# Performance work log

Hardware: AMD Instinct MI355X
Metric: run time of the kernel (lower is better)

## Reference

```python
import jax, jax.numpy as jnp
import numpy as np

HEADS = 8
DIM_HEAD = 64
SCALE = DIM_HEAD ** -0.5


def setup_inputs() -> dict:
    key = jax.random.key(0)
    ks = jax.random.split(key, 8)
    B, Nq, Dq = 4, 2048, 512
    Nk, Dc = 1024, 768
    inner = HEADS * DIM_HEAD  # 512
    x = jax.random.normal(ks[0], (B, Nq, Dq), dtype=jnp.float32)
    context = jax.random.normal(ks[1], (B, Nk, Dc), dtype=jnp.float32)
    # Linear weights stored [in, out]; y = x @ W (+ b)
    Wq = jax.random.normal(ks[2], (Dq, inner), dtype=jnp.float32) / np.sqrt(Dq)
    Wk = jax.random.normal(ks[3], (Dc, inner), dtype=jnp.float32) / np.sqrt(Dc)
    Wv = jax.random.normal(ks[4], (Dc, inner), dtype=jnp.float32) / np.sqrt(Dc)
    Wo = jax.random.normal(ks[5], (inner, Dq), dtype=jnp.float32) / np.sqrt(inner)
    bo = jax.random.normal(ks[6], (Dq,), dtype=jnp.float32) * 0.01
    return {"x": x, "context": context, "Wq": Wq, "Wk": Wk, "Wv": Wv, "Wo": Wo, "bo": bo}


def reference(x, context, Wq, Wk, Wv, Wo, bo):
    B, Nq, _ = x.shape
    Nk = context.shape[1]
    # projections
    q = x @ Wq          # [B, Nq, h*d]
    k = context @ Wk    # [B, Nk, h*d]
    v = context @ Wv    # [B, Nk, h*d]
    # split heads: b n (h d) -> b h n d
    q = q.reshape(B, Nq, HEADS, DIM_HEAD).transpose(0, 2, 1, 3)
    k = k.reshape(B, Nk, HEADS, DIM_HEAD).transpose(0, 2, 1, 3)
    v = v.reshape(B, Nk, HEADS, DIM_HEAD).transpose(0, 2, 1, 3)
    # fp32 QK^T (ATTN_PRECISION == 'fp32' path)
    sim = jnp.einsum('bhid,bhjd->bhij', q.astype(jnp.float32), k.astype(jnp.float32)) * SCALE
    attn = jax.nn.softmax(sim, axis=-1)
    out = jnp.einsum('bhij,bhjd->bhid', attn, v)  # [B, h, Nq, d]
    out = out.transpose(0, 2, 1, 3).reshape(B, Nq, HEADS * DIM_HEAD)
    return out @ Wo + bo  # dropout=0 -> identity
```

## Files before the change

kernel.cpp:

```cpp
#include <hip/hip_runtime.h>
#include <cstddef>
#include <cstdint>

typedef __attribute__((ext_vector_type(8))) short bf16x8;
typedef __attribute__((ext_vector_type(4))) float f32x4;

static __device__ __forceinline__ short f2bf(float f) {
    union { float f; unsigned u; } x;
    x.f = f;
    unsigned r = (x.u + 0x7FFFu + ((x.u >> 16) & 1u)) >> 16;
    return (short)r;
}

typedef __attribute__((address_space(3))) unsigned lds_u;
typedef const __attribute__((address_space(1))) unsigned glb_u;
static __device__ __forceinline__ void gld_lds16(const void* g, void* l) {
    __builtin_amdgcn_global_load_lds((glb_u*)g, (lds_u*)l, 16, 0, 0);
}

__global__ __launch_bounds__(256) void convert_kernel(
    const float* __restrict__ x, const float* __restrict__ c,
    short* __restrict__ xb, short* __restrict__ cb, int n1, int n2)
{
    int i = blockIdx.x * 256 + threadIdx.x;
    int nn1 = n1 >> 2;
    const float* src; short* dst; int off;
    if (i < nn1) { src = x; dst = xb; off = i; }
    else { src = c; dst = cb; off = i - nn1; if (off >= (n2 >> 2)) return; }
    float4 v = ((const float4*)src)[off];
    ushort4 w;
    w.x = (unsigned short)f2bf(v.x); w.y = (unsigned short)f2bf(v.y);
    w.z = (unsigned short)f2bf(v.z); w.w = (unsigned short)f2bf(v.w);
    ((ushort4*)dst)[off] = w;
}

__global__ __launch_bounds__(256) void wtrans_kernel(
    const float* __restrict__ Wq, const float* __restrict__ Wk,
    const float* __restrict__ Wv, const float* __restrict__ Wo,
    short* __restrict__ wqT, short* __restrict__ wkvT, short* __restrict__ woT)
{
    __shared__ float T[32][33];
    const int z = blockIdx.z;
    const float* src; short* dst; int R;
    if (z == 0)      { src = Wq; dst = wqT;  R = 512; }
    else if (z == 1) { src = Wk; dst = wkvT; R = 768; }
    else if (z == 2) { src = Wv; dst = wkvT + (size_t)512 * 768; R = 768; }
    else             { src = Wo; dst = woT;  R = 512; }
    const int yt = blockIdx.y;
    if (yt * 32 >= R) return;
    const int xt = blockIdx.x;
    const int tid = threadIdx.x;
    {
        int r = tid >> 3, c4 = (tid & 7) * 4;
        float4 v = *(const float4*)&src[(size_t)(yt * 32 + r) * 512 + xt * 32 + c4];
        T[r][c4] = v.x; T[r][c4 + 1] = v.y; T[r][c4 + 2] = v.z; T[r][c4 + 3] = v.w;
    }
    __syncthreads();
    {
        int cc = tid >> 3, r4 = (tid & 7) * 4;
        ushort4 w;
        w.x = (unsigned short)f2bf(T[r4][cc]);     w.y = (unsigned short)f2bf(T[r4 + 1][cc]);
        w.z = (unsigned short)f2bf(T[r4 + 2][cc]); w.w = (unsigned short)f2bf(T[r4 + 3][cc]);
        *(ushort4*)&dst[(size_t)(xt * 32 + cc) * R + yt * 32 + r4] = w;
    }
}

__global__ __launch_bounds__(256) void vtrans_kernel(
    const short* __restrict__ v, short* __restrict__ vT)
{
    __shared__ short T[32][33];
    const int b = blockIdx.z, yt = blockIdx.y, xt = blockIdx.x;
    const int tid = threadIdx.x;
    {
        int r = tid >> 3, c4 = (tid & 7) * 4;
        ushort4 vv = *(const ushort4*)&v[((size_t)(b * 1024 + yt * 32 + r)) * 1024 + xt * 32 + c4];
        T[r][c4] = (short)vv.x; T[r][c4 + 1] = (short)vv.y;
        T[r][c4 + 2] = (short)vv.z; T[r][c4 + 3] = (short)vv.w;
    }
    __syncthreads();
    {
        int cc = tid >> 3, r4 = (tid & 7) * 4;
        ushort4 w;
        w.x = (unsigned short)T[r4][cc];     w.y = (unsigned short)T[r4 + 1][cc];
        w.z = (unsigned short)T[r4 + 2][cc]; w.w = (unsigned short)T[r4 + 3][cc];
        int kk = yt * 32 + r4;
        int kl = kk & 63;
        int g  = ((kl >> 5) << 2) | ((kl >> 2) & 3);
        int p  = (kk & ~63) | (g << 3) | (((kl >> 4) & 1) << 2);
        *(ushort4*)&vT[((size_t)(b * 512 + xt * 32 + cc)) * 1024 + p] = w;
    }
}

static __device__ __forceinline__ void gemm_core(
    const short* __restrict__ A, const short* __restrict__ BT, int K,
    int bm, int bn, short* As, short* Bs, f32x4 acc[4][4])
{
    const int tid  = threadIdx.x;
    const int lane = tid & 63;
    const int wave = tid >> 6;
    const int lm   = lane & 15;
    const int quad = lane >> 4;
    const int wm = (wave >> 1) * 64;
    const int wn = (wave & 1) * 64;
    const int c = tid >> 7, r = tid & 127;

    {
        const short* Ag = &A[(size_t)(bm + r) * K];
        const short* Bg = &BT[(size_t)(bn + r) * K];
        gld_lds16(Ag + c * 8,       &As[tid * 8]);
        gld_lds16(Ag + (c + 2) * 8, &As[(tid + 256) * 8]);
        gld_lds16(Bg + c * 8,       &Bs[tid * 8]);
        gld_lds16(Bg + (c + 2) * 8, &Bs[(tid + 256) * 8]);
    }

    for (int k0 = 0, it = 0; k0 < K; k0 += 32, ++it) {
        short* Ac = As + (it & 1) * 4096;
        short* Bc = Bs + (it & 1) * 4096;
        __syncthreads();
        if (k0 + 32 < K) {
            short* An = As + ((it & 1) ^ 1) * 4096;
            short* Bn = Bs + ((it & 1) ^ 1) * 4096;
            const short* Ag = &A[(size_t)(bm + r) * K + k0 + 32];
            const short* Bg = &BT[(size_t)(bn + r) * K + k0 + 32];
            gld_lds16(Ag + c * 8,       &An[tid * 8]);
            gld_lds16(Ag + (c + 2) * 8, &An[(tid + 256) * 8]);
            gld_lds16(Bg + c * 8,       &Bn[tid * 8]);
            gld_lds16(Bg + (c + 2) * 8, &Bn[(tid + 256) * 8]);
        }
        bf16x8 af[4], bfr[4];
        #pragma unroll
        for (int i = 0; i < 4; ++i)
            af[i] = *(const bf16x8*)&Ac[(quad * 128 + wm + i * 16 + lm) * 8];
        #pragma unroll
        for (int j = 0; j < 4; ++j)
            bfr[j] = *(const bf16x8*)&Bc[(quad * 128 + wn + j * 16 + lm) * 8];
        #pragma unroll
        for (int i = 0; i < 4; ++i)
            #pragma unroll
            for (int j = 0; j < 4; ++j)
                acc[i][j] = __builtin_amdgcn_mfma_f32_16x16x32_bf16(
                    af[i], bfr[j], acc[i][j], 0, 0, 0);
    }
}

__global__ __launch_bounds__(256) void qkv_kernel(
    const short* __restrict__ xb, const short* __restrict__ cb,
    const short* __restrict__ wqT, const short* __restrict__ wkvT,
    short* __restrict__ qb, short* __restrict__ kvb)
{
    __shared__ short As[2 * 4096];
    __shared__ short Bs[2 * 4096];
    const int bid = blockIdx.x;
    const short *A, *BT; short* C; int K, ldc, bm, bn; float cscale;
    if (bid < 256) { A = xb; BT = wqT;  C = qb;  K = 512; ldc = 512;
                     bm = (bid >> 2) * 128; bn = (bid & 3) * 128;
                     cscale = 0.18033688f; }
    else { int b2 = bid - 256; A = cb; BT = wkvT; C = kvb; K = 768; ldc = 1024;
           bm = (b2 >> 3) * 128; bn = (b2 & 7) * 128; cscale = 1.0f; }

    f32x4 acc[4][4] = {};
    gemm_core(A, BT, K, bm, bn, As, Bs, acc);

    const int lane = threadIdx.x & 63, wave = threadIdx.x >> 6;
    const int lm = lane & 15, quad = lane >> 4;
    const int wm = (wave >> 1) * 64, wn = (wave & 1) * 64;
    #pragma unroll
    for (int j = 0; j < 4; ++j) {
        int col = bn + wn + j * 16 + lm;
        #pragma unroll
        for (int i = 0; i < 4; ++i) {
            int row0 = bm + wm + i * 16 + quad * 4;
            #pragma unroll
            for (int r = 0; r < 4; ++r)
                C[(size_t)(row0 + r) * ldc + col] = f2bf(acc[i][j][r] * cscale);
        }
    }
}

__global__ __launch_bounds__(256) void ogemm_kernel(
    const short* __restrict__ ob, const short* __restrict__ woT,
    const float* __restrict__ bias, float* __restrict__ out)
{
    __shared__ short As[2 * 4096];
    __shared__ short Bs[2 * 4096];
    const int bid = blockIdx.x;
    const int bm = (bid >> 2) * 128, bn = (bid & 3) * 128;

    f32x4 acc[4][4] = {};
    gemm_core(ob, woT, 512, bm, bn, As, Bs, acc);

    const int lane = threadIdx.x & 63, wave = threadIdx.x >> 6;
    const int lm = lane & 15, quad = lane >> 4;
    const int wm = (wave >> 1) * 64, wn = (wave & 1) * 64;
    #pragma unroll
    for (int j = 0; j < 4; ++j) {
        int col = bn + wn + j * 16 + lm;
        float bv = bias[col];
        #pragma unroll
        for (int i = 0; i < 4; ++i) {
            int row0 = bm + wm + i * 16 + quad * 4;
            #pragma unroll
            for (int r = 0; r < 4; ++r)
                out[(size_t)(row0 + r) * 512 + col] = acc[i][j][r] + bv;
        }
    }
}

__global__ __launch_bounds__(256) void attn_kernel(
    const short* __restrict__ q, const short* __restrict__ k,
    const short* __restrict__ vT, short* __restrict__ o)
{
    __shared__ short Ks[3 * 4096];
    __shared__ short Vs[3 * 4096];

    const int tid  = threadIdx.x;
    const int lane = tid & 63;
    const int wave = tid >> 6;
    const int lm   = lane & 15;
    const int quad = lane >> 4;

    const int bid = blockIdx.x;
    const int xcdq = bid >> 3;
    const int hb = (bid & 7) + ((xcdq >> 5) << 3);
    const int qt = xcdq & 31;
    const int h = hb & 7, b = hb >> 3;

    const size_t qrow0 = (size_t)b * 2048 + qt * 64;
    const size_t krow0 = (size_t)b * 1024;
    const int hcol = h * 64;
    const size_t vrow0 = ((size_t)b * 8 + h) * 64;

    const short* kg = &k[(krow0 + (tid & 63)) * 1024 + hcol + (tid >> 6) * 8];
    const short* vg = &vT[(vrow0 + (tid & 63)) * 1024 + (tid >> 6) * 8];

    const short* qrow = &q[(qrow0 + wave * 16 + lm) * 512 + hcol];
    bf16x8 qf0 = *(const bf16x8*)&qrow[quad * 8];
    bf16x8 qf1 = *(const bf16x8*)&qrow[32 + quad * 8];
    asm volatile("" :: "v"(qf0), "v"(qf1));

    gld_lds16(kg,      &Ks[tid * 8]);
    gld_lds16(kg + 32, &Ks[(tid + 256) * 8]);
    gld_lds16(vg,      &Vs[tid * 8]);
    gld_lds16(vg + 32, &Vs[(tid + 256) * 8]);
    kg += 64 * 1024; vg += 64;
    gld_lds16(kg,      &Ks[4096 + tid * 8]);
    gld_lds16(kg + 32, &Ks[4096 + (tid + 256) * 8]);
    gld_lds16(vg,      &Vs[4096 + tid * 8]);
    gld_lds16(vg + 32, &Vs[4096 + (tid + 256) * 8]);
    kg += 64 * 1024; vg += 64;

    f32x4 oacc[4] = {};
    float lsum = 0.0f;
    const int fro = (quad * 64 + lm) * 8;

    int ocur = 0;
    int onxt = 2 * 4096;
    for (int t = 0; t < 16; ++t) {
        if (t < 15) asm volatile("s_waitcnt vmcnt(4)" ::: "memory");
        else        asm volatile("s_waitcnt vmcnt(0)" ::: "memory");
        __builtin_amdgcn_s_barrier();
        __builtin_amdgcn_sched_barrier(0);
        if (t < 14) {
            gld_lds16(kg,      &Ks[onxt + tid * 8]);
            gld_lds16(kg + 32, &Ks[onxt + (tid + 256) * 8]);
            gld_lds16(vg,      &Vs[onxt + tid * 8]);
            gld_lds16(vg + 32, &Vs[onxt + (tid + 256) * 8]);
            kg += 64 * 1024; vg += 64;
        }
        const short* Kc = &Ks[ocur + fro];
        const short* Vc = &Vs[ocur + fro];

        f32x4 sacc[4] = {};
        __builtin_amdgcn_s_setprio(1);
        #pragma unroll
        for (int j = 0; j < 4; ++j) {
            bf16x8 kf0 = *(const bf16x8*)&Kc[(j * 16) * 8];
            bf16x8 kf1 = *(const bf16x8*)&Kc[(256 + j * 16) * 8];
            sacc[j] = __builtin_amdgcn_mfma_f32_16x16x32_bf16(kf0, qf0, sacc[j], 0, 0, 0);
            sacc[j] = __builtin_amdgcn_mfma_f32_16x16x32_bf16(kf1, qf1, sacc[j], 0, 0, 0);
        }
        __builtin_amdgcn_s_setprio(0);

        union { unsigned u[4]; bf16x8 v; } pf0, pf1;
        #pragma unroll
        for (int j = 0; j < 4; ++j) {
            #pragma unroll
            for (int rp = 0; rp < 2; ++rp) {
                float p0 = __builtin_amdgcn_exp2f(sacc[j][2 * rp]);
                float p1 = __builtin_amdgcn_exp2f(sacc[j][2 * rp + 1]);
                lsum += p0 + p1;
                unsigned pr;
                asm("v_cvt_pk_bf16_f32 %0, %1, %2" : "=v"(pr) : "v"(p0), "v"(p1));
                if (j < 2) pf0.u[j * 2 + rp] = pr;
                else       pf1.u[(j - 2) * 2 + rp] = pr;
            }
        }

        __builtin_amdgcn_s_setprio(1);
        #pragma unroll
        for (int j = 0; j < 4; ++j) {
            bf16x8 vf0 = *(const bf16x8*)&Vc[(j * 16) * 8];
            bf16x8 vf1 = *(const bf16x8*)&Vc[(256 + j * 16) * 8];
            oacc[j] = __builtin_amdgcn_mfma_f32_16x16x32_bf16(pf0.v, vf0, oacc[j], 0, 0, 0);
            oacc[j] = __builtin_amdgcn_mfma_f32_16x16x32_bf16(pf1.v, vf1, oacc[j], 0, 0, 0);
        }
        __builtin_amdgcn_s_setprio(0);

        ocur += 4096; if (ocur == 12288) ocur = 0;
        onxt += 4096; if (onxt == 12288) onxt = 0;
    }

    float s = lsum;
    s += __shfl_xor(s, 16);
    s += __shfl_xor(s, 32);
    const float inv = 1.0f / s;
    float invr[4];
    #pragma unroll
    for (int r = 0; r < 4; ++r)
        invr[r] = __shfl(inv, quad * 20 + r);

    #pragma unroll
    for (int j = 0; j < 4; ++j) {
        int col = hcol + j * 16 + lm;
        #pragma unroll
        for (int r = 0; r < 4; ++r) {
            size_t row = qrow0 + wave * 16 + quad * 4 + r;
            o[row * 512 + col] = f2bf(oacc[j][r] * invr[r]);
        }
    }
}

extern "C" void kernel_launch(void* const* d_in, const int* in_sizes, int n_in,
                              void* d_out, int out_size, void* d_ws, size_t ws_size,
                              hipStream_t stream)
{
    const float* x   = (const float*)d_in[0];
    const float* ctx = (const float*)d_in[1];
    const float* Wq  = (const float*)d_in[2];
    const float* Wk  = (const float*)d_in[3];
    const float* Wv  = (const float*)d_in[4];
    const float* Wo  = (const float*)d_in[5];
    const float* bo  = (const float*)d_in[6];

    char* ws = (char*)d_ws;
    short* xb   = (short*)(ws);
    short* cb   = (short*)(ws + (8u << 20));
    short* wqT  = (short*)(ws + (14u << 20));
    short* wkvT = (short*)(ws + (14u << 20) + (512u << 10));
    short* woT  = (short*)(ws + (16u << 20));
    short* qb   = (short*)(ws + (16u << 20) + (512u << 10));
    short* kvb  = (short*)(ws + (24u << 20) + (512u << 10));
    short* ob   = xb;
    short* vT   = cb;

    convert_kernel<<<7168, 256, 0, stream>>>(x, ctx, xb, cb, 8192 * 512, 4096 * 768);
    wtrans_kernel<<<dim3(16, 24, 4), 256, 0, stream>>>(Wq, Wk, Wv, Wo, wqT, wkvT, woT);
    qkv_kernel<<<512, 256, 0, stream>>>(xb, cb, wqT, wkvT, qb, kvb);
    vtrans_kernel<<<dim3(16, 32, 4), 256, 0, stream>>>(kvb + 512, vT);
    attn_kernel<<<1024, 256, 0, stream>>>(qb, kvb, vT, ob);
    ogemm_kernel<<<256, 256, 0, stream>>>(ob, woT, bo, (float*)d_out);
}
```

Before: 188.2 us.

## Process two query row tiles per wave in attention to reuse K/V fragments

```diff
diff --git a/kernel.cpp b/kernel.cpp
--- a/kernel.cpp
+++ b/kernel.cpp
@@ -221,11 +221,11 @@
 
     const int bid = blockIdx.x;
     const int xcdq = bid >> 3;
-    const int hb = (bid & 7) + ((xcdq >> 5) << 3);
-    const int qt = xcdq & 31;
+    const int hb = (bid & 7) + ((xcdq >> 4) << 3);
+    const int qt = xcdq & 15;
     const int h = hb & 7, b = hb >> 3;
 
-    const size_t qrow0 = (size_t)b * 2048 + qt * 64;
+    const size_t qrow0 = (size_t)b * 2048 + qt * 128;
     const size_t krow0 = (size_t)b * 1024;
     const int hcol = h * 64;
     const size_t vrow0 = ((size_t)b * 8 + h) * 64;
@@ -233,10 +233,13 @@
     const short* kg = &k[(krow0 + (tid & 63)) * 1024 + hcol + (tid >> 6) * 8];
     const short* vg = &vT[(vrow0 + (tid & 63)) * 1024 + (tid >> 6) * 8];
 
-    const short* qrow = &q[(qrow0 + wave * 16 + lm) * 512 + hcol];
-    bf16x8 qf0 = *(const bf16x8*)&qrow[quad * 8];
-    bf16x8 qf1 = *(const bf16x8*)&qrow[32 + quad * 8];
-    asm volatile("" :: "v"(qf0), "v"(qf1));
+    const short* qrow0p = &q[(qrow0 + wave * 32 + lm) * 512 + hcol];
+    const short* qrow1p = qrow0p + 16 * 512;
+    bf16x8 qf00 = *(const bf16x8*)&qrow0p[quad * 8];
+    bf16x8 qf01 = *(const bf16x8*)&qrow0p[32 + quad * 8];
+    bf16x8 qf10 = *(const bf16x8*)&qrow1p[quad * 8];
+    bf16x8 qf11 = *(const bf16x8*)&qrow1p[32 + quad * 8];
+    asm volatile("" :: "v"(qf00), "v"(qf01), "v"(qf10), "v"(qf11));
 
     gld_lds16(kg,      &Ks[tid * 8]);
     gld_lds16(kg + 32, &Ks[(tid + 256) * 8]);
@@ -249,8 +252,8 @@
     gld_lds16(vg + 32, &Vs[4096 + (tid + 256) * 8]);
     kg += 64 * 1024; vg += 64;
 
-    f32x4 oacc[4] = {};
-    float lsum = 0.0f;
+    f32x4 oacc[2][4] = {};
+    float lsum[2] = {0.0f, 0.0f};
     const int fro = (quad * 64 + lm) * 8;
 
     int ocur = 0;
@@ -270,29 +273,35 @@
         const short* Kc = &Ks[ocur + fro];
         const short* Vc = &Vs[ocur + fro];
 
-        f32x4 sacc[4] = {};
+        f32x4 sacc0[4] = {}, sacc1[4] = {};
         __builtin_amdgcn_s_setprio(1);
         #pragma unroll
         for (int j = 0; j < 4; ++j) {
             bf16x8 kf0 = *(const bf16x8*)&Kc[(j * 16) * 8];
             bf16x8 kf1 = *(const bf16x8*)&Kc[(256 + j * 16) * 8];
-            sacc[j] = __builtin_amdgcn_mfma_f32_16x16x32_bf16(kf0, qf0, sacc[j], 0, 0, 0);
-            sacc[j] = __builtin_amdgcn_mfma_f32_16x16x32_bf16(kf1, qf1, sacc[j], 0, 0, 0);
+            sacc0[j] = __builtin_amdgcn_mfma_f32_16x16x32_bf16(kf0, qf00, sacc0[j], 0, 0, 0);
+            sacc1[j] = __builtin_amdgcn_mfma_f32_16x16x32_bf16(kf0, qf10, sacc1[j], 0, 0, 0);
+            sacc0[j] = __builtin_amdgcn_mfma_f32_16x16x32_bf16(kf1, qf01, sacc0[j], 0, 0, 0);
+            sacc1[j] = __builtin_amdgcn_mfma_f32_16x16x32_bf16(kf1, qf11, sacc1[j], 0, 0, 0);
         }
         __builtin_amdgcn_s_setprio(0);
 
-        union { unsigned u[4]; bf16x8 v; } pf0, pf1;
+        union { unsigned u[4]; bf16x8 v; } pf00, pf01, pf10, pf11;
         #pragma unroll
         for (int j = 0; j < 4; ++j) {
             #pragma unroll
             for (int rp = 0; rp < 2; ++rp) {
-                float p0 = __builtin_amdgcn_exp2f(sacc[j][2 * rp]);
-                float p1 = __builtin_amdgcn_exp2f(sacc[j][2 * rp + 1]);
-                lsum += p0 + p1;
-                unsigned pr;
-                asm("v_cvt_pk_bf16_f32 %0, %1, %2" : "=v"(pr) : "v"(p0), "v"(p1));
-                if (j < 2) pf0.u[j * 2 + rp] = pr;
-                else       pf1.u[(j - 2) * 2 + rp] = pr;
+                float a0 = __builtin_amdgcn_exp2f(sacc0[j][2 * rp]);
+                float a1 = __builtin_amdgcn_exp2f(sacc0[j][2 * rp + 1]);
+                float b0 = __builtin_amdgcn_exp2f(sacc1[j][2 * rp]);
+                float b1 = __builtin_amdgcn_exp2f(sacc1[j][2 * rp + 1]);
+                lsum[0] += a0 + a1;
+                lsum[1] += b0 + b1;
+                unsigned pa, pb;
+                asm("v_cvt_pk_bf16_f32 %0, %1, %2" : "=v"(pa) : "v"(a0), "v"(a1));
+                asm("v_cvt_pk_bf16_f32 %0, %1, %2" : "=v"(pb) : "v"(b0), "v"(b1));
+                if (j < 2) { pf00.u[j * 2 + rp] = pa; pf10.u[j * 2 + rp] = pb; }
+                else       { pf01.u[(j - 2) * 2 + rp] = pa; pf11.u[(j - 2) * 2 + rp] = pb; }
             }
         }
 
@@ -301,8 +310,10 @@
         for (int j = 0; j < 4; ++j) {
             bf16x8 vf0 = *(const bf16x8*)&Vc[(j * 16) * 8];
             bf16x8 vf1 = *(const bf16x8*)&Vc[(256 + j * 16) * 8];
-            oacc[j] = __builtin_amdgcn_mfma_f32_16x16x32_bf16(pf0.v, vf0, oacc[j], 0, 0, 0);
-            oacc[j] = __builtin_amdgcn_mfma_f32_16x16x32_bf16(pf1.v, vf1, oacc[j], 0, 0, 0);
+            oacc[0][j] = __builtin_amdgcn_mfma_f32_16x16x32_bf16(pf00.v, vf0, oacc[0][j], 0, 0, 0);
+            oacc[1][j] = __builtin_amdgcn_mfma_f32_16x16x32_bf16(pf10.v, vf0, oacc[1][j], 0, 0, 0);
+            oacc[0][j] = __builtin_amdgcn_mfma_f32_16x16x32_bf16(pf01.v, vf1, oacc[0][j], 0, 0, 0);
+            oacc[1][j] = __builtin_amdgcn_mfma_f32_16x16x32_bf16(pf11.v, vf1, oacc[1][j], 0, 0, 0);
         }
         __builtin_amdgcn_s_setprio(0);
 
@@ -310,22 +321,24 @@
         onxt += 4096; if (onxt == 12288) onxt = 0;
     }
 
-    float s = lsum;
-    s += __shfl_xor(s, 16);
-    s += __shfl_xor(s, 32);
-    const float inv = 1.0f / s;
-    float invr[4];
     #pragma unroll
-    for (int r = 0; r < 4; ++r)
-        invr[r] = __shfl(inv, quad * 20 + r);
-
-    #pragma unroll
-    for (int j = 0; j < 4; ++j) {
-        int col = hcol + j * 16 + lm;
-        #pragma unroll
-        for (int r = 0; r < 4; ++r) {
-            size_t row = qrow0 + wave * 16 + quad * 4 + r;
-            o[row * 512 + col] = f2bf(oacc[j][r] * invr[r]);
+    for (int g = 0; g < 2; ++g) {
+        float s = lsum[g];
+        s += __shfl_xor(s, 16);
+        s += __shfl_xor(s, 32);
+        const float inv = 1.0f / s;
+        float invr[4];
+        #pragma unroll
+        for (int r = 0; r < 4; ++r)
+            invr[r] = __shfl(inv, quad * 20 + r);
+        #pragma unroll
+        for (int j = 0; j < 4; ++j) {
+            int col = hcol + j * 16 + lm;
+            #pragma unroll
+            for (int r = 0; r < 4; ++r) {
+                size_t row = qrow0 + wave * 32 + g * 16 + quad * 4 + r;
+                o[row * 512 + col] = f2bf(oacc[g][j][r] * invr[r]);
+            }
         }
     }
 }
@@ -357,6 +370,6 @@
     wtrans_kernel<<<dim3(16, 24, 4), 256, 0, stream>>>(Wq, Wk, Wv, Wo, wqT, wkvT, woT);
     qkv_kernel<<<512, 256, 0, stream>>>(xb, cb, wqT, wkvT, qb, kvb);
     vtrans_kernel<<<dim3(16, 32, 4), 256, 0, stream>>>(kvb + 512, vT);
-    attn_kernel<<<1024, 256, 0, stream>>>(qb, kvb, vT, ob);
+    attn_kernel<<<512, 256, 0, stream>>>(qb, kvb, vT, ob);
     ogemm_kernel<<<256, 256, 0, stream>>>(ob, woT, bo, (float*)d_out);
 }
```

After: 173.9 us. 1.08x faster.
